# Kernel tuning notes

Measured on AMD Instinct MI355X. Metric: run time of the kernel, lower is better.

## Reference

```python
import jax, jax.numpy as jnp
import numpy as np

IN_F, OUT_F, K, STRIDE, PAD = 256, 256, 3, 1, 1
SEARCH_SPACE = (2, 4, 8, 16)  # derived in __init__ from in/out=256, feature_size=16


def _cir_project(weight, b):
    """Circulant projection of conv weight for block size b.
    Equivalent to the nested diagonal-mean + roll loops in trans_to_cir:
      tc[q,p,i] = mean_j tmp[q,p,j,(j+i)%b]   (wrapped diagonal mean)
      w[q,p,r,c] = tc[q,p,(r-c)%b]            (roll construction)
    """
    q, p = OUT_F // b, IN_F // b
    tmp = weight.reshape(q, b, p, b, K, K).transpose(0, 2, 1, 3, 4, 5)  # (q,p,b,b,k,k)
    j = jnp.arange(b)
    diag_idx = (j[:, None] + j[None, :]) % b          # (b_j, b_i)
    tc = tmp[:, :, j[:, None], diag_idx].mean(axis=2)  # (q,p,b,k,k)
    circ_idx = (j[:, None] - j[None, :]) % b          # (r, c)
    w = tc[:, :, circ_idx]                             # (q,p,b,b,k,k)
    return w.transpose(0, 2, 1, 3, 4, 5).reshape(OUT_F, IN_F, K, K)


def setup_inputs() -> dict:
    key = jax.random.key(0)
    k1, k2 = jax.random.split(key, 2)
    x = jax.random.normal(k1, (256, IN_F, 16, 16), jnp.float32)
    weight = jax.random.normal(k2, (OUT_F, IN_F, K, K), jnp.float32) * 0.05
    alphas = jnp.ones((len(SEARCH_SPACE) + 1,), jnp.float32)
    return {"x": x, "weight": weight, "alphas": alphas}


def reference(x, weight, alphas):
    # gumbel_softmax with finetune=False -> plain softmax over alphas
    a = jax.nn.softmax(alphas)
    w = a[0] * weight
    for i, b in enumerate(SEARCH_SPACE):
        w = w + a[i + 1] * _cir_project(weight, b)
    return jax.lax.conv_general_dilated(
        x, w,
        window_strides=(STRIDE, STRIDE),
        padding=[(PAD, PAD), (PAD, PAD)],
        dimension_numbers=("NCHW", "OIHW", "NCHW"),
    )
```

## Files before the change

kernel.cpp:

```cpp
#include <hip/hip_runtime.h>
#include <cstdint>
#include <cstddef>

#define NIMG 256
#define PADW 18
#define XB_IMG (PADW * PADW * 256)
#define W2_ROW 2304

typedef __bf16 bf16x8 __attribute__((ext_vector_type(8)));
typedef float floatx4 __attribute__((ext_vector_type(4)));

__device__ __forceinline__ unsigned short f2bf(float f) {
    unsigned u = __float_as_uint(f);
    u = (u + 0x7FFFu + ((u >> 16) & 1u)) >> 16;
    return (unsigned short)u;
}

__device__ __forceinline__ void gload_lds16(const void* g, void* l) {
    __builtin_amdgcn_global_load_lds(
        (const __attribute__((address_space(1))) void*)g,
        (__attribute__((address_space(3))) void*)l, 16, 0, 0);
}

__global__ __launch_bounds__(256) void convert_kernel(
        const float* __restrict__ x, unsigned short* __restrict__ xb) {
    __shared__ __align__(16) unsigned short tile[256][66];
    const int n  = blockIdx.x;
    const int c0 = blockIdx.y * 64;
    const int t  = threadIdx.x;
    const float* xi = x + (size_t)n * 65536;
    unsigned short* xo = xb + (size_t)n * XB_IMG;

    if (blockIdx.y == 0) {
        for (int idx = t; idx < 68 * 128; idx += 256) {
            int hp = idx >> 7;
            int c2 = (idx & 127) * 2;
            int py, px;
            if (hp < 18)      { py = 0;       px = hp;      }
            else if (hp < 36) { py = 17;      px = hp - 18; }
            else if (hp < 52) { py = hp - 35; px = 0;       }
            else              { py = hp - 51; px = 17;      }
            *(unsigned int*)&xo[(py * 18 + px) * 256 + c2] = 0u;
        }
    }

    #pragma unroll 4
    for (int i = 0; i < 64; ++i) {
        float v = xi[(c0 + i) * 256 + t];
        tile[t][i] = f2bf(v);
    }
    __syncthreads();

    #pragma unroll
    for (int it = 0; it < 32; ++it) {
        int idx = it * 256 + t;
        int p   = idx >> 5;
        int c2  = (idx & 31) * 2;
        unsigned int v = *(const unsigned int*)&tile[p][c2];
        int py = (p >> 4) + 1, px = (p & 15) + 1;
        *(unsigned int*)&xo[(py * 18 + px) * 256 + c0 + c2] = v;
    }
}

__global__ __launch_bounds__(256) void wprep_kernel(
        const float* __restrict__ wt, const float* __restrict__ alphas,
        unsigned short* __restrict__ w2) {
    __shared__ float wlds[16][257];
    const int o16 = blockIdx.x * 16;
    const int pos = blockIdx.y;
    const int t   = threadIdx.x;

    #pragma unroll
    for (int j = 0; j < 16; ++j)
        wlds[j][t] = wt[((o16 + j) * 256 + t) * 9 + pos];

    float a[5];
    {
        float mx = alphas[0];
        #pragma unroll
        for (int i = 1; i < 5; ++i) mx = fmaxf(mx, alphas[i]);
        float s = 0.f;
        #pragma unroll
        for (int i = 0; i < 5; ++i) { a[i] = __expf(alphas[i] - mx); s += a[i]; }
        float inv = 1.f / s;
        #pragma unroll
        for (int i = 0; i < 5; ++i) a[i] *= inv;
    }
    __syncthreads();

    const int c = t;
    #pragma unroll
    for (int oo = 0; oo < 16; ++oo) {
        float acc = a[0] * wlds[oo][c];
        #pragma unroll
        for (int bi = 0; bi < 4; ++bi) {
            const int b  = 2 << bi;
            const int r  = oo & (b - 1);
            const int cc = c & (b - 1);
            const int i0 = (r - cc) & (b - 1);
            const int ob = oo - r;
            const int icb = c - cc;
            float s2 = 0.f;
            for (int j = 0; j < b; ++j)
                s2 += wlds[ob + j][icb + ((j + i0) & (b - 1))];
            acc += a[1 + bi] * s2 * (1.f / (float)b);
        }
        w2[(size_t)(o16 + oo) * W2_ROW + pos * 256 + c] = f2bf(acc);
    }
}

__global__ __launch_bounds__(256) void gemm_kernel(
        const unsigned short* __restrict__ xb,
        const unsigned short* __restrict__ w2,
        float* __restrict__ out) {
    __shared__ __align__(16) unsigned short xs[128 * 64];
    __shared__ __align__(16) unsigned short ws[128 * 64];

    const int t    = threadIdx.x;
    const int lane = t & 63;
    const int wid  = t >> 6;

    const int b     = blockIdx.x;
    const int s_    = b >> 3;
    const int ptile = (b & 7) * 64 + (s_ >> 1);
    const int ktile = s_ & 1;
    const int n_img = ptile >> 1;
    const int half  = ptile & 1;
    const int kbase = ktile * 128;

    const int rlo  = lane >> 3;
    const int cswz = ((lane & 7) - rlo) & 7;
    const int coff = cswz * 8;

    int xg[8], wg[8];
    {
        const int sub = wid & 1;
        #pragma unroll
        for (int i = 0; i < 8; ++i) {
            int r = sub * 64 + i * 8 + rlo;
            int y  = half * 8 + (r >> 4);
            int xq = r & 15;
            xg[i] = n_img * XB_IMG + ((y + 1) * 18 + (xq + 1)) * 256 + coff;
            int kr = kbase + sub * 64 + i * 8 + rlo;
            wg[i] = kr * W2_ROW + coff;
        }
    }
    const int lds_base = (wid & 1) * 4096;

    const floatx4 z4 = {0.f, 0.f, 0.f, 0.f};
    floatx4 acc[4][4];
    #pragma unroll
    for (int i = 0; i < 4; ++i)
        #pragma unroll
        for (int j = 0; j < 4; ++j) acc[i][j] = z4;

    const int wrow = wid >> 1, wcol = wid & 1;
    const int arow = wrow * 64 + (lane & 15);
    const int brow = wcol * 64 + (lane & 15);
    const int sa0  = (arow + (lane >> 4)) & 7;
    const int sb0  = (brow + (lane >> 4)) & 7;

    for (int pos = 0; pos < 9; ++pos) {
        const int dp = ((pos / 3) - 1) * (18 * 256) + ((pos % 3) - 1) * 256;
        #pragma unroll
        for (int cs = 0; cs < 4; ++cs) {
            __syncthreads();
            if (wid < 2) {
                const int go = dp + cs * 64;
                #pragma unroll
                for (int i = 0; i < 8; ++i)
                    gload_lds16(xb + xg[i] + go, &xs[lds_base + i * 512]);
            } else {
                const int go = pos * 256 + cs * 64;
                #pragma unroll
                for (int i = 0; i < 8; ++i)
                    gload_lds16(w2 + wg[i] + go, &ws[lds_base + i * 512]);
            }
            __syncthreads();

            #pragma unroll
            for (int ks = 0; ks < 2; ++ks) {
                const int sa = (sa0 + ks * 4) & 7;
                const int sb = (sb0 + ks * 4) & 7;
                bf16x8 af[4], bfr[4];
                #pragma unroll
                for (int mt = 0; mt < 4; ++mt)
                    af[mt] = *(const bf16x8*)&ws[(arow + mt * 16) * 64 + sa * 8];
                #pragma unroll
                for (int nt = 0; nt < 4; ++nt)
                    bfr[nt] = *(const bf16x8*)&xs[(brow + nt * 16) * 64 + sb * 8];
                #pragma unroll
                for (int mt = 0; mt < 4; ++mt)
                    #pragma unroll
                    for (int nt = 0; nt < 4; ++nt)
                        acc[mt][nt] = __builtin_amdgcn_mfma_f32_16x16x32_bf16(
                            af[mt], bfr[nt], acc[mt][nt], 0, 0, 0);
            }
        }
    }

    const int p0 = half * 128 + wcol * 64;
    const int k0 = kbase + wrow * 64;
    float* ob = out + (size_t)n_img * 65536;
    #pragma unroll
    for (int mt = 0; mt < 4; ++mt) {
        #pragma unroll
        for (int nt = 0; nt < 4; ++nt) {
            const int kout = k0 + mt * 16 + (lane >> 4) * 4;
            const int p    = p0 + nt * 16 + (lane & 15);
            #pragma unroll
            for (int r = 0; r < 4; ++r)
                ob[(kout + r) * 256 + p] = acc[mt][nt][r];
        }
    }
}

__global__ __launch_bounds__(256) void naive_conv(
        const float* __restrict__ x, const unsigned short* __restrict__ w2,
        float* __restrict__ out) {
    __shared__ float wr[2304];
    const int n = blockIdx.x >> 8, k = blockIdx.x & 255;
    const int t = threadIdx.x;
    for (int i = t; i < 2304; i += 256)
        wr[i] = __uint_as_float(((unsigned)w2[k * W2_ROW + i]) << 16);
    __syncthreads();
    const int y = t >> 4, xx = t & 15;
    const float* xi = x + (size_t)n * 65536;
    float acc = 0.f;
    for (int pos = 0; pos < 9; ++pos) {
        int dy = pos / 3 - 1, dx = pos % 3 - 1;
        int yy = y + dy, x2 = xx + dx;
        if (yy < 0 || yy > 15 || x2 < 0 || x2 > 15) continue;
        const float* xp = xi + yy * 16 + x2;
        const float* wp = wr + pos * 256;
        for (int c = 0; c < 256; ++c) acc += xp[c * 256] * wp[c];
    }
    out[(size_t)n * 65536 + k * 256 + t] = acc;
}

extern "C" void kernel_launch(void* const* d_in, const int* in_sizes, int n_in,
                              void* d_out, int out_size, void* d_ws, size_t ws_size,
                              hipStream_t stream) {
    const float* x      = (const float*)d_in[0];
    const float* wt     = (const float*)d_in[1];
    const float* alphas = (const float*)d_in[2];
    float* out = (float*)d_out;

    const size_t xb_elems = (size_t)NIMG * XB_IMG;
    const size_t w2_elems = (size_t)256 * W2_ROW;
    const size_t need = (xb_elems + w2_elems) * sizeof(unsigned short);

    if (ws_size >= need) {
        unsigned short* xb = (unsigned short*)d_ws;
        unsigned short* w2 = xb + xb_elems;
        convert_kernel<<<dim3(256, 4), 256, 0, stream>>>(x, xb);
        wprep_kernel<<<dim3(16, 9), 256, 0, stream>>>(wt, alphas, w2);
        gemm_kernel<<<dim3(1024), 256, 0, stream>>>(xb, w2, out);
    } else if (ws_size >= w2_elems * sizeof(unsigned short)) {
        unsigned short* w2 = (unsigned short*)d_ws;
        wprep_kernel<<<dim3(16, 9), 256, 0, stream>>>(wt, alphas, w2);
        naive_conv<<<dim3(256 * 256), 256, 0, stream>>>(x, w2, out);
    }
}
```

Before: 214.9 us.

## Switch conv GEMM to 32x32x16 MFMA and vectorize input conversion

The main conv kernel now uses 32x32x16 bf16 MFMA tiles (2x2 per wave) in place of 16x16x32 tiles (4x4 per wave). This halves the LDS fragment loads per k-step and uses the larger MFMA shape, which gives more work per instruction. The epilogue is remapped to the 32x32 output layout. Separately, the convert kernel reads x with float4 loads into a channel-major LDS tile and zeroes the halo with 8-byte stores. The new LDS read pattern in the transpose may cause bank conflicts.

Result: slower. 236.6 us (+10.1%).

```diff
diff --git a/kernel.cpp b/kernel.cpp
--- a/kernel.cpp
+++ b/kernel.cpp
@@ -9,6 +9,8 @@
 
 typedef __bf16 bf16x8 __attribute__((ext_vector_type(8)));
 typedef float floatx4 __attribute__((ext_vector_type(4)));
+typedef float floatx16 __attribute__((ext_vector_type(16)));
+typedef float floatvec4 __attribute__((ext_vector_type(4)));
 
 __device__ __forceinline__ unsigned short f2bf(float f) {
     unsigned u = __float_as_uint(f);
@@ -24,7 +26,7 @@
 
 __global__ __launch_bounds__(256) void convert_kernel(
         const float* __restrict__ x, unsigned short* __restrict__ xb) {
-    __shared__ __align__(16) unsigned short tile[256][66];
+    __shared__ __align__(16) unsigned short tile2[64][268];
     const int n  = blockIdx.x;
     const int c0 = blockIdx.y * 64;
     const int t  = threadIdx.x;
@@ -32,22 +34,31 @@
     unsigned short* xo = xb + (size_t)n * XB_IMG;
 
     if (blockIdx.y == 0) {
-        for (int idx = t; idx < 68 * 128; idx += 256) {
-            int hp = idx >> 7;
-            int c2 = (idx & 127) * 2;
+        #pragma unroll
+        for (int it = 0; it < 17; ++it) {
+            int idx = it * 256 + t;
+            int hp = idx >> 6;
+            int c4 = (idx & 63) * 4;
             int py, px;
             if (hp < 18)      { py = 0;       px = hp;      }
             else if (hp < 36) { py = 17;      px = hp - 18; }
             else if (hp < 52) { py = hp - 35; px = 0;       }
             else              { py = hp - 51; px = 17;      }
-            *(unsigned int*)&xo[(py * 18 + px) * 256 + c2] = 0u;
-        }
-    }
-
-    #pragma unroll 4
-    for (int i = 0; i < 64; ++i) {
-        float v = xi[(c0 + i) * 256 + t];
-        tile[t][i] = f2bf(v);
+            *(uint2*)&xo[(py * 18 + px) * 256 + c4] = make_uint2(0u, 0u);
+        }
+    }
+
+    {
+        const int p4 = (t & 63) * 4;
+        const int ci = t >> 6;
+        #pragma unroll
+        for (int i = 0; i < 16; ++i) {
+            const int c = i * 4 + ci;
+            floatvec4 v = *(const floatvec4*)&xi[(c0 + c) * 256 + p4];
+            unsigned lo = (unsigned)f2bf(v.x) | ((unsigned)f2bf(v.y) << 16);
+            unsigned hi = (unsigned)f2bf(v.z) | ((unsigned)f2bf(v.w) << 16);
+            *(uint2*)&tile2[c][p4] = make_uint2(lo, hi);
+        }
     }
     __syncthreads();
 
@@ -55,10 +66,11 @@
     for (int it = 0; it < 32; ++it) {
         int idx = it * 256 + t;
         int p   = idx >> 5;
-        int c2  = (idx & 31) * 2;
-        unsigned int v = *(const unsigned int*)&tile[p][c2];
+        int cp  = (idx & 31) * 2;
+        unsigned lo = tile2[cp][p];
+        unsigned hi = tile2[cp + 1][p];
         int py = (p >> 4) + 1, px = (p & 15) + 1;
-        *(unsigned int*)&xo[(py * 18 + px) * 256 + c0 + c2] = v;
+        *(unsigned int*)&xo[(py * 18 + px) * 256 + c0 + cp] = lo | (hi << 16);
     }
 }
 
@@ -147,18 +159,20 @@
     }
     const int lds_base = (wid & 1) * 4096;
 
-    const floatx4 z4 = {0.f, 0.f, 0.f, 0.f};
-    floatx4 acc[4][4];
-    #pragma unroll
-    for (int i = 0; i < 4; ++i)
-        #pragma unroll
-        for (int j = 0; j < 4; ++j) acc[i][j] = z4;
+    floatx16 acc[2][2];
+    #pragma unroll
+    for (int i = 0; i < 2; ++i)
+        #pragma unroll
+        for (int j = 0; j < 2; ++j)
+            #pragma unroll
+            for (int r = 0; r < 16; ++r) acc[i][j][r] = 0.f;
 
     const int wrow = wid >> 1, wcol = wid & 1;
-    const int arow = wrow * 64 + (lane & 15);
-    const int brow = wcol * 64 + (lane & 15);
-    const int sa0  = (arow + (lane >> 4)) & 7;
-    const int sb0  = (brow + (lane >> 4)) & 7;
+    const int l31  = lane & 31, lhi = lane >> 5;
+    const int ar   = wrow * 64 + l31;
+    const int br   = wcol * 64 + l31;
+    const int sa0  = (ar + lhi) & 7;
+    const int sb0  = (br + lhi) & 7;
 
     for (int pos = 0; pos < 9; ++pos) {
         const int dp = ((pos / 3) - 1) * (18 * 256) + ((pos % 3) - 1) * 256;
@@ -179,22 +193,20 @@
             __syncthreads();
 
             #pragma unroll
-            for (int ks = 0; ks < 2; ++ks) {
-                const int sa = (sa0 + ks * 4) & 7;
-                const int sb = (sb0 + ks * 4) & 7;
-                bf16x8 af[4], bfr[4];
+            for (int ks = 0; ks < 4; ++ks) {
+                const int sa = (sa0 + ks * 2) & 7;
+                const int sb = (sb0 + ks * 2) & 7;
+                bf16x8 af[2], bf[2];
+                af[0] = *(const bf16x8*)&ws[ar * 64 + sa * 8];
+                af[1] = *(const bf16x8*)&ws[(ar + 32) * 64 + sa * 8];
+                bf[0] = *(const bf16x8*)&xs[br * 64 + sb * 8];
+                bf[1] = *(const bf16x8*)&xs[(br + 32) * 64 + sb * 8];
                 #pragma unroll
-                for (int mt = 0; mt < 4; ++mt)
-                    af[mt] = *(const bf16x8*)&ws[(arow + mt * 16) * 64 + sa * 8];
-                #pragma unroll
-                for (int nt = 0; nt < 4; ++nt)
-                    bfr[nt] = *(const bf16x8*)&xs[(brow + nt * 16) * 64 + sb * 8];
-                #pragma unroll
-                for (int mt = 0; mt < 4; ++mt)
+                for (int mt = 0; mt < 2; ++mt)
                     #pragma unroll
-                    for (int nt = 0; nt < 4; ++nt)
-                        acc[mt][nt] = __builtin_amdgcn_mfma_f32_16x16x32_bf16(
-                            af[mt], bfr[nt], acc[mt][nt], 0, 0, 0);
+                    for (int nt = 0; nt < 2; ++nt)
+                        acc[mt][nt] = __builtin_amdgcn_mfma_f32_32x32x16_bf16(
+                            af[mt], bf[nt], acc[mt][nt], 0, 0, 0);
             }
         }
     }
@@ -203,14 +215,15 @@
     const int k0 = kbase + wrow * 64;
     float* ob = out + (size_t)n_img * 65536;
     #pragma unroll
-    for (int mt = 0; mt < 4; ++mt) {
-        #pragma unroll
-        for (int nt = 0; nt < 4; ++nt) {
-            const int kout = k0 + mt * 16 + (lane >> 4) * 4;
-            const int p    = p0 + nt * 16 + (lane & 15);
+    for (int mt = 0; mt < 2; ++mt) {
+        #pragma unroll
+        for (int nt = 0; nt < 2; ++nt) {
+            const int p = p0 + nt * 32 + l31;
             #pragma unroll
-            for (int r = 0; r < 4; ++r)
-                ob[(kout + r) * 256 + p] = acc[mt][nt][r];
+            for (int r = 0; r < 16; ++r) {
+                const int kout = k0 + mt * 32 + (r & 3) + 8 * (r >> 2) + 4 * lhi;
+                ob[kout * 256 + p] = acc[mt][nt][r];
+            }
         }
     }
 }
```

## Double-buffer GEMM LDS tiles and vectorize input conversion loads

Applied to the files above, without the earlier changes.

The GEMM main loop is flattened into 36 steps with two LDS buffers per operand. Each step prefetches the next x/w tile with global_load_lds while MFMAs consume the current one, which removes one barrier per step and overlaps global-load latency with compute. The input conversion kernel now reads float4 vectors and uses a channel-major LDS tile with 8-byte writes, and the border zeroing uses wider stores. The cost is doubled LDS per GEMM block, which may reduce occupancy, and 2-byte strided LDS reads in the transpose stage.

Result: slower. 449.4 us (+109.1%).

```diff
diff --git a/kernel.cpp b/kernel.cpp
--- a/kernel.cpp
+++ b/kernel.cpp
@@ -9,6 +9,7 @@
 
 typedef __bf16 bf16x8 __attribute__((ext_vector_type(8)));
 typedef float floatx4 __attribute__((ext_vector_type(4)));
+typedef float floatvec4 __attribute__((ext_vector_type(4)));
 
 __device__ __forceinline__ unsigned short f2bf(float f) {
     unsigned u = __float_as_uint(f);
@@ -24,7 +25,7 @@
 
 __global__ __launch_bounds__(256) void convert_kernel(
         const float* __restrict__ x, unsigned short* __restrict__ xb) {
-    __shared__ __align__(16) unsigned short tile[256][66];
+    __shared__ __align__(16) unsigned short tile2[64][268];
     const int n  = blockIdx.x;
     const int c0 = blockIdx.y * 64;
     const int t  = threadIdx.x;
@@ -32,22 +33,31 @@
     unsigned short* xo = xb + (size_t)n * XB_IMG;
 
     if (blockIdx.y == 0) {
-        for (int idx = t; idx < 68 * 128; idx += 256) {
-            int hp = idx >> 7;
-            int c2 = (idx & 127) * 2;
+        #pragma unroll
+        for (int it = 0; it < 17; ++it) {
+            int idx = it * 256 + t;
+            int hp = idx >> 6;
+            int c4 = (idx & 63) * 4;
             int py, px;
             if (hp < 18)      { py = 0;       px = hp;      }
             else if (hp < 36) { py = 17;      px = hp - 18; }
             else if (hp < 52) { py = hp - 35; px = 0;       }
             else              { py = hp - 51; px = 17;      }
-            *(unsigned int*)&xo[(py * 18 + px) * 256 + c2] = 0u;
-        }
-    }
-
-    #pragma unroll 4
-    for (int i = 0; i < 64; ++i) {
-        float v = xi[(c0 + i) * 256 + t];
-        tile[t][i] = f2bf(v);
+            *(uint2*)&xo[(py * 18 + px) * 256 + c4] = make_uint2(0u, 0u);
+        }
+    }
+
+    {
+        const int p4 = (t & 63) * 4;
+        const int ci = t >> 6;
+        #pragma unroll
+        for (int i = 0; i < 16; ++i) {
+            const int c = i * 4 + ci;
+            floatvec4 v = *(const floatvec4*)&xi[(c0 + c) * 256 + p4];
+            unsigned lo = (unsigned)f2bf(v.x) | ((unsigned)f2bf(v.y) << 16);
+            unsigned hi = (unsigned)f2bf(v.z) | ((unsigned)f2bf(v.w) << 16);
+            *(uint2*)&tile2[c][p4] = make_uint2(lo, hi);
+        }
     }
     __syncthreads();
 
@@ -55,10 +65,11 @@
     for (int it = 0; it < 32; ++it) {
         int idx = it * 256 + t;
         int p   = idx >> 5;
-        int c2  = (idx & 31) * 2;
-        unsigned int v = *(const unsigned int*)&tile[p][c2];
+        int cp  = (idx & 31) * 2;
+        unsigned lo = tile2[cp][p];
+        unsigned hi = tile2[cp + 1][p];
         int py = (p >> 4) + 1, px = (p & 15) + 1;
-        *(unsigned int*)&xo[(py * 18 + px) * 256 + c0 + c2] = v;
+        *(unsigned int*)&xo[(py * 18 + px) * 256 + c0 + cp] = lo | (hi << 16);
     }
 }
 
@@ -113,8 +124,8 @@
         const unsigned short* __restrict__ xb,
         const unsigned short* __restrict__ w2,
         float* __restrict__ out) {
-    __shared__ __align__(16) unsigned short xs[128 * 64];
-    __shared__ __align__(16) unsigned short ws[128 * 64];
+    __shared__ __align__(16) unsigned short xs[2][8192];
+    __shared__ __align__(16) unsigned short ws[2][8192];
 
     const int t    = threadIdx.x;
     const int lane = t & 63;
@@ -160,42 +171,46 @@
     const int sa0  = (arow + (lane >> 4)) & 7;
     const int sb0  = (brow + (lane >> 4)) & 7;
 
-    for (int pos = 0; pos < 9; ++pos) {
-        const int dp = ((pos / 3) - 1) * (18 * 256) + ((pos % 3) - 1) * 256;
-        #pragma unroll
-        for (int cs = 0; cs < 4; ++cs) {
-            __syncthreads();
-            if (wid < 2) {
-                const int go = dp + cs * 64;
-                #pragma unroll
-                for (int i = 0; i < 8; ++i)
-                    gload_lds16(xb + xg[i] + go, &xs[lds_base + i * 512]);
-            } else {
-                const int go = pos * 256 + cs * 64;
-                #pragma unroll
-                for (int i = 0; i < 8; ++i)
-                    gload_lds16(w2 + wg[i] + go, &ws[lds_base + i * 512]);
-            }
-            __syncthreads();
-
-            #pragma unroll
-            for (int ks = 0; ks < 2; ++ks) {
-                const int sa = (sa0 + ks * 4) & 7;
-                const int sb = (sb0 + ks * 4) & 7;
-                bf16x8 af[4], bfr[4];
-                #pragma unroll
-                for (int mt = 0; mt < 4; ++mt)
-                    af[mt] = *(const bf16x8*)&ws[(arow + mt * 16) * 64 + sa * 8];
+    auto issue = [&](int st, int pp) {
+        const int pos = st >> 2;
+        const int cs  = st & 3;
+        if (wid < 2) {
+            const int dy = pos / 3, dx = pos - dy * 3;
+            const int go = (dy - 1) * (18 * 256) + (dx - 1) * 256 + cs * 64;
+            #pragma unroll
+            for (int i = 0; i < 8; ++i)
+                gload_lds16(xb + xg[i] + go, &xs[pp][lds_base + i * 512]);
+        } else {
+            const int go = pos * 256 + cs * 64;
+            #pragma unroll
+            for (int i = 0; i < 8; ++i)
+                gload_lds16(w2 + wg[i] + go, &ws[pp][lds_base + i * 512]);
+        }
+    };
+
+    issue(0, 0);
+    for (int step = 0; step < 36; ++step) {
+        const int pp = step & 1;
+        __syncthreads();
+        if (step + 1 < 36) issue(step + 1, pp ^ 1);
+
+        #pragma unroll
+        for (int ks = 0; ks < 2; ++ks) {
+            const int sa = (sa0 + ks * 4) & 7;
+            const int sb = (sb0 + ks * 4) & 7;
+            bf16x8 af[4], bfr[4];
+            #pragma unroll
+            for (int mt = 0; mt < 4; ++mt)
+                af[mt] = *(const bf16x8*)&ws[pp][(arow + mt * 16) * 64 + sa * 8];
+            #pragma unroll
+            for (int nt = 0; nt < 4; ++nt)
+                bfr[nt] = *(const bf16x8*)&xs[pp][(brow + nt * 16) * 64 + sb * 8];
+            #pragma unroll
+            for (int mt = 0; mt < 4; ++mt)
                 #pragma unroll
                 for (int nt = 0; nt < 4; ++nt)
-                    bfr[nt] = *(const bf16x8*)&xs[(brow + nt * 16) * 64 + sb * 8];
-                #pragma unroll
-                for (int mt = 0; mt < 4; ++mt)
-                    #pragma unroll
-                    for (int nt = 0; nt < 4; ++nt)
-                        acc[mt][nt] = __builtin_amdgcn_mfma_f32_16x16x32_bf16(
-                            af[mt], bfr[nt], acc[mt][nt], 0, 0, 0);
-            }
+                    acc[mt][nt] = __builtin_amdgcn_mfma_f32_16x16x32_bf16(
+                        af[mt], bfr[nt], acc[mt][nt], 0, 0, 0);
         }
     }
 
```
